# Kernel optimization log

Measured on AMD Instinct MI355X. Metric: run time of the kernel, lower is better.

## Reference

```python
import jax, jax.numpy as jnp
import numpy as np

B, T, FD, NH, NC, NOUT = 32, 512, 256, 1024, 512, 8


def setup_inputs() -> dict:
    key = jax.random.key(0)
    ks = jax.random.split(key, 12)
    s = lambda k, sh, sc=0.05: (jax.random.normal(k, sh, jnp.float32) * sc)
    return dict(
        x=jax.random.normal(ks[0], (B, T, FD), jnp.float32),
        lens=jax.random.randint(ks[1], (B,), T // 2, T + 1, jnp.int32),
        W1=s(ks[2], (NH, FD)), b1=jnp.zeros((NH,), jnp.float32),
        g1=jnp.ones((NH,), jnp.float32), be1=jnp.zeros((NH,), jnp.float32),
        W2=s(ks[3], (NH, NH)), b2=jnp.zeros((NH,), jnp.float32),
        g2=jnp.ones((NH,), jnp.float32), be2=jnp.zeros((NH,), jnp.float32),
        lstm_wih=s(ks[4], (2, 2, 4 * NC, NH)),   # [layer, dir, 4H, in]
        lstm_whh=s(ks[5], (2, 2, 4 * NC, NC)),   # [layer, dir, 4H, H]
        lstm_bih=s(ks[6], (2, 2, 4 * NC)),
        lstm_bhh=s(ks[7], (2, 2, 4 * NC)),
        w_u=s(ks[8], (2 * NC,)), b_u=jnp.zeros((), jnp.float32),
        Wc=s(ks[9], (NOUT, 2 * NC)), bc=jnp.zeros((NOUT,), jnp.float32),
    )


def _layernorm(x, g, b, eps=1e-5):
    m = x.mean(-1, keepdims=True)
    v = ((x - m) ** 2).mean(-1, keepdims=True)
    return (x - m) / jnp.sqrt(v + eps) * g + b


def _lrelu(z):
    return jnp.where(z >= 0, z, 0.01 * z)  # LeakyReLU default slope


def _lstm_dir(x, wih, whh, bih, bhh):
    # x: [B,T,in] -> h: [B,T,H]; torch gate order i,f,g,o
    Bz = x.shape[0]
    H = whh.shape[1]
    xp = jnp.einsum('bti,gi->btg', x, wih) + bih + bhh  # [B,T,4H]

    def step(carry, xt):
        h, c = carry
        gates = xt + h @ whh.T
        i, f, g, o = jnp.split(gates, 4, axis=-1)
        c = jax.nn.sigmoid(f) * c + jax.nn.sigmoid(i) * jnp.tanh(g)
        h = jax.nn.sigmoid(o) * jnp.tanh(c)
        return (h, c), h

    h0 = jnp.zeros((Bz, H), x.dtype)
    _, hs = jax.lax.scan(step, (h0, h0), xp.transpose(1, 0, 2))
    return hs.transpose(1, 0, 2)


def _bilstm(x, wih, whh, bih, bhh):
    # params indexed [dir, ...]; backward dir processes the full padded
    # sequence reversed (original feeds unpacked pad_sequence to nn.LSTM)
    hf = _lstm_dir(x, wih[0], whh[0], bih[0], bhh[0])
    hb = _lstm_dir(x[:, ::-1], wih[1], whh[1], bih[1], bhh[1])[:, ::-1]
    return jnp.concatenate([hf, hb], axis=-1)


def reference(x, lens, W1, b1, g1, be1, W2, b2, g2, be2,
              lstm_wih, lstm_whh, lstm_bih, lstm_bhh, w_u, b_u, Wc, bc):
    Tn = x.shape[1]
    # extract MLP (dropout = identity in eval)
    h = _lrelu(_layernorm(x @ W1.T + b1, g1, be1))
    h = _lrelu(_layernorm(h @ W2.T + b2, g2, be2))
    # pad_sequence zero-pads AFTER extract -> zero out pad positions
    mask = jnp.arange(Tn)[None, :] < lens[:, None]  # [B,T]
    h = h * mask[..., None]
    # 2-layer bidirectional LSTM over the full padded sequence
    h = _bilstm(h, lstm_wih[0], lstm_whh[0], lstm_bih[0], lstm_bhh[0])
    h = _bilstm(h, lstm_wih[1], lstm_whh[1], lstm_bih[1], lstm_bhh[1])
    # Attn with window_len=1: per-step linear score, masked softmax, weighted sum
    scores = h @ w_u + b_u                          # [B,T]
    scores = jnp.where(mask, scores, -jnp.inf)
    alpha = jax.nn.softmax(scores, axis=-1)
    pooled = jnp.einsum('bt,btd->bd', alpha, h)     # [B, 2*NC]
    return pooled @ Wc.T + bc
```

## Files before the change

kernel.cpp:

```cpp
#include <hip/hip_runtime.h>
#include <stdint.h>
#include <stddef.h>


typedef short  short8  __attribute__((ext_vector_type(8)));
typedef short  short4v __attribute__((ext_vector_type(4)));
typedef float  float4v __attribute__((ext_vector_type(4)));
typedef unsigned long long u64;

__device__ inline float b2f(short x){
  union { unsigned u; float f; } v; v.u = ((unsigned)(unsigned short)x) << 16; return v.f;
}
__device__ inline short f2b(float f){
  union { float f; unsigned u; } v; v.f = f;
  unsigned r = (v.u + 0x7fffu + ((v.u >> 16) & 1u)) >> 16;
  return (short)r;
}
__device__ inline float sigm(float x){ return 1.f / (1.f + __expf(-x)); }
__device__ inline float tanh_(float x){ return 2.f / (1.f + __expf(-2.f*x)) - 1.f; }

__global__ __launch_bounds__(256) void detect_f32(
    const unsigned short* __restrict__ p, unsigned* __restrict__ flag)
{
  const int tid = threadIdx.x;
  unsigned h = 0;
  for (int i = tid; i < 1024; i += 256){
    const unsigned e = (p[i] >> 7) & 0xFFu;
    if (e >= 0xC0u) ++h;
  }
#pragma unroll
  for (int off=32; off>0; off>>=1) h += __shfl_xor(h, off, 64);
  __shared__ unsigned sh[4];
  if ((tid&63)==0) sh[tid>>6] = h;
  __syncthreads();
  if (tid==0) *flag = (sh[0]+sh[1]+sh[2]+sh[3] >= 8u) ? 1u : 0u;
}

struct CvtArgs {
  const void* src[16];
  short*      dst[16];
  int         n[16];
  int         boff[17];
};

__global__ __launch_bounds__(256) void to_bf16_batch(
    CvtArgs a, const unsigned* __restrict__ flag)
{
  const int b = blockIdx.x;
  int lo = 0, hi = 15;
  while (lo < hi){
    const int mid = (lo + hi + 1) >> 1;
    if (b >= a.boff[mid]) lo = mid; else hi = mid - 1;
  }
  const int i   = lo;
  const int idx = (b - a.boff[i])*256 + (int)threadIdx.x;
  if (idx >= a.n[i]) return;
  if (*flag) a.dst[i][idx] = f2b(((const float*)a.src[i])[idx]);
  else       a.dst[i][idx] = ((const short*)a.src[i])[idx];
}

__global__ __launch_bounds__(256) void gemm_bt(
    const short* __restrict__ A, const short* __restrict__ W,
    short* __restrict__ C, const short* __restrict__ bias1,
    const short* __restrict__ bias2, int N, int K)
{
  __shared__ __align__(16) short lA[128*40];
  __shared__ __align__(16) short lW[128*40];
  const int tid  = threadIdx.x;
  const int lane = tid & 63, wv = tid >> 6;
  const int wm = wv >> 1, wn = wv & 1;
  const int quad = lane >> 4, l15 = lane & 15;

  const int gx  = gridDim.x;
  const int nwg = gx * gridDim.y;
  int flat = blockIdx.x + blockIdx.y * gx;
  if ((nwg & 7) == 0){
    const int cpx = nwg >> 3;
    flat = (flat & 7)*cpx + (flat >> 3);
  }
  const long m0 = (long)(flat / gx) * 128, n0 = (long)(flat % gx) * 128;

  float4v acc[4][4];
#pragma unroll
  for (int i=0;i<4;++i)
#pragma unroll
    for (int j=0;j<4;++j) acc[i][j] = (float4v)0.f;

  const int r  = tid >> 2;
  const int kc = tid & 3;
  const int nkt = K >> 5;
  for (int kt = 0; kt < nkt; ++kt) {
    __syncthreads();
    const short* ga = A + (m0 + r) * (long)K + kt*32 + kc*8;
    const short* gw = W + (n0 + r) * (long)K + kt*32 + kc*8;
    short8 a0 = *(const short8*)ga;
    short8 a1 = *(const short8*)(ga + 64*(long)K);
    short8 w0 = *(const short8*)gw;
    short8 w1 = *(const short8*)(gw + 64*(long)K);
    *(short8*)&lA[r*40 + kc*8]        = a0;
    *(short8*)&lA[(r+64)*40 + kc*8]   = a1;
    *(short8*)&lW[r*40 + kc*8]        = w0;
    *(short8*)&lW[(r+64)*40 + kc*8]   = w1;
    __syncthreads();
    short8 af[4], bfr[4];
#pragma unroll
    for (int i=0;i<4;++i) af[i]  = *(const short8*)&lA[(wm*64 + i*16 + l15)*40 + quad*8];
#pragma unroll
    for (int j=0;j<4;++j) bfr[j] = *(const short8*)&lW[(wn*64 + j*16 + l15)*40 + quad*8];
#pragma unroll
    for (int i=0;i<4;++i)
#pragma unroll
      for (int j=0;j<4;++j)
        acc[i][j] = __builtin_amdgcn_mfma_f32_16x16x32_bf16(af[i], bfr[j], acc[i][j], 0, 0, 0);
  }
#pragma unroll
  for (int j=0;j<4;++j){
    const long n = n0 + wn*64 + j*16 + l15;
    float bs = b2f(bias1[n]);
    if (bias2) bs += b2f(bias2[n]);
#pragma unroll
    for (int i=0;i<4;++i){
      const long mb = m0 + wm*64 + i*16 + quad*4;
#pragma unroll
      for (int g=0; g<4; ++g)
        C[(mb+g)*(long)N + n] = f2b(acc[i][j][g] + bs);
    }
  }
}

__global__ __launch_bounds__(256) void ln_lrelu(
    const short* __restrict__ X, const short* __restrict__ g,
    const short* __restrict__ be, short* __restrict__ out,
    const int* __restrict__ lens, const int domask)
{
  const int row = blockIdx.x, tid = threadIdx.x;
  const short* xr = X + (size_t)row * 1024;
  short4v xv = *(const short4v*)(xr + tid*4);
  float v[4];
#pragma unroll
  for (int k=0;k<4;++k) v[k] = b2f(xv[k]);
  float s  = v[0]+v[1]+v[2]+v[3];
  float sq = v[0]*v[0]+v[1]*v[1]+v[2]*v[2]+v[3]*v[3];
#pragma unroll
  for (int off=32; off>0; off>>=1){
    s  += __shfl_xor(s,  off, 64);
    sq += __shfl_xor(sq, off, 64);
  }
  __shared__ float red[8];
  if ((tid&63)==0){ red[tid>>6] = s; red[4+(tid>>6)] = sq; }
  __syncthreads();
  s  = red[0]+red[1]+red[2]+red[3];
  sq = red[4]+red[5]+red[6]+red[7];
  const float mean = s * (1.f/1024.f);
  const float var  = sq * (1.f/1024.f) - mean*mean;
  const float rstd = rsqrtf(var + 1e-5f);
  float zmul = 1.f;
  if (domask){ const int b = row >> 9, t = row & 511; if (t >= lens[b]) zmul = 0.f; }
  short4v o;
#pragma unroll
  for (int k=0;k<4;++k){
    const int n = tid*4 + k;
    float y = (v[k]-mean)*rstd*b2f(g[n]) + b2f(be[n]);
    y = (y >= 0.f) ? y : 0.01f*y;
    o[k] = f2b(y * zmul);
  }
  *(short4v*)(out + (size_t)row*1024 + tid*4) = o;
}

__global__ __launch_bounds__(256) void lstm_scan(
    const short* __restrict__ xp, const int xp_cols, const int dir0,
    const short* __restrict__ whh,
    u64* __restrict__ hstate,
    short* __restrict__ hout,
    const unsigned epoch)
{
  const int wg = blockIdx.x;
  const int dloc = wg >> 5, d = dir0 + dloc;
  const int u0 = (wg & 31) * 16;
  const int tid = threadIdx.x, lane = tid & 63, wv = tid >> 6;
  const int quad = lane >> 4, l15 = lane & 15;

  short8 af[16];
  {
    const short* wr = whh + ((size_t)d*2048 + wv*512 + u0 + l15)*512 + quad*8;
#pragma unroll
    for (int ks=0; ks<16; ++ks) af[ks] = *(const short8*)(wr + ks*32);
  }

  const int bb = tid >> 3, pp = tid & 7;
  float cstA = 0.f, cstB = 0.f;
  __shared__ __align__(16) unsigned hsh[2][32*260];
  __shared__ float gl[4][16][33];
  const unsigned tbase = epoch << 10;

  for (int step=0; step<512; ++step){
    const int t = d ? (511-step) : step;
    short4v x0, x1;
    {
      const size_t gb = (size_t)dloc*2048 + (size_t)wv*512 + u0 + quad*4;
      x0 = *(const short4v*)(xp + ((size_t)l15*512      + t)*xp_cols + gb);
      x1 = *(const short4v*)(xp + ((size_t)(l15+16)*512 + t)*xp_cols + gb);
    }
    unsigned* stg = &hsh[step&1][tid];
    if (step == 0){
#pragma unroll
      for (int k=0;k<32;++k) stg[k*260] = 0u;
    } else {
      const u64* hq = hstate + ((size_t)(d*2 + (step&1))<<13) + tid;
      const unsigned tgt = tbase + (unsigned)step;
      u64 v[32];
      for(;;){
        unsigned ok = 1u;
#pragma unroll
        for (int k=0;k<32;++k)
          v[k] = __hip_atomic_load(hq + (size_t)k*256,
                                   __ATOMIC_RELAXED, __HIP_MEMORY_SCOPE_AGENT);
#pragma unroll
        for (int k=0;k<32;++k) ok &= (unsigned)((unsigned)(v[k] >> 32) == tgt);
        if (ok) break;
        __builtin_amdgcn_s_sleep(1);
      }
#pragma unroll
      for (int k=0;k<32;++k) stg[k*260] = (unsigned)v[k];
    }
    __syncthreads();

    float4v acc0, acc1;
#pragma unroll
    for (int g=0; g<4; ++g){ acc0[g] = b2f(x0[g]); acc1[g] = b2f(x1[g]); }
    const short* hs = (const short*)&hsh[step&1][0];
#pragma unroll
    for (int ks=0; ks<16; ++ks){
      short8 b0 = *(const short8*)(hs + (size_t)l15*520      + ks*32 + quad*8);
      short8 b1 = *(const short8*)(hs + (size_t)(l15+16)*520 + ks*32 + quad*8);
      acc0 = __builtin_amdgcn_mfma_f32_16x16x32_bf16(af[ks], b0, acc0, 0, 0, 0);
      acc1 = __builtin_amdgcn_mfma_f32_16x16x32_bf16(af[ks], b1, acc1, 0, 0, 0);
    }
#pragma unroll
    for (int g=0; g<4; ++g){
      gl[wv][quad*4+g][l15]    = acc0[g];
      gl[wv][quad*4+g][l15+16] = acc1[g];
    }
    __syncthreads();

    float hv[2];
#pragma unroll
    for (int i=0; i<2; ++i){
      const int uu = 2*pp + i;
      const float gi = gl[0][uu][bb], gf = gl[1][uu][bb];
      const float gg = gl[2][uu][bb], go = gl[3][uu][bb];
      float& cref = i ? cstB : cstA;
      const float c = sigm(gf)*cref + sigm(gi)*tanh_(gg);
      cref = c;
      hv[i] = sigm(go) * tanh_(c);
    }
    const unsigned hw = (unsigned)(unsigned short)f2b(hv[0])
                      | ((unsigned)(unsigned short)f2b(hv[1]) << 16);
    const u64 pkt = ((u64)(tbase + (unsigned)step + 1u) << 32) | (u64)hw;
    __hip_atomic_store(hstate + ((size_t)(d*2 + ((step+1)&1))<<13)
                         + (size_t)bb*256 + (u0>>1) + pp,
                       pkt, __ATOMIC_RELAXED, __HIP_MEMORY_SCOPE_AGENT);
    *(unsigned*)&hout[((size_t)bb*512 + t)*1024 + d*512 + u0 + 2*pp] = hw;
  }
}

__global__ __launch_bounds__(256) void attn_cls(
    const short* __restrict__ hseq, const short* __restrict__ wu,
    const short* __restrict__ Wc, const short* __restrict__ bc,
    const int* __restrict__ lens, float* __restrict__ out)
{
  const int b = blockIdx.x, tid = threadIdx.x, lane = tid & 63, wv = tid >> 6;
  const int len = lens[b];
  __shared__ float wus[1024];
  __shared__ float sc[512];
  __shared__ float redx[8];
  __shared__ float pooled[1024];
  for (int i=tid; i<1024; i+=256) wus[i] = b2f(wu[i]);
  __syncthreads();
  const short* hb = hseq + (size_t)b*512*1024;
  for (int t=wv; t<512; t+=4){
    const short* hr = hb + (size_t)t*1024;
    float s = 0.f;
#pragma unroll
    for (int j=0;j<16;++j) s += b2f(hr[lane + j*64]) * wus[lane + j*64];
#pragma unroll
    for (int off=32; off>0; off>>=1) s += __shfl_xor(s, off, 64);
    if (lane==0) sc[t] = (t < len) ? s : -3.0e38f;
  }
  __syncthreads();
  float m = -3.0e38f;
  for (int i=tid;i<512;i+=256) m = fmaxf(m, sc[i]);
#pragma unroll
  for (int off=32; off>0; off>>=1) m = fmaxf(m, __shfl_xor(m, off, 64));
  if (lane==0) redx[wv] = m;
  __syncthreads();
  m = fmaxf(fmaxf(redx[0],redx[1]), fmaxf(redx[2],redx[3]));
  float ssum = 0.f;
  for (int i=tid;i<512;i+=256){
    float e = (i<len) ? __expf(sc[i]-m) : 0.f;
    sc[i] = e;
    ssum += e;
  }
#pragma unroll
  for (int off=32; off>0; off>>=1) ssum += __shfl_xor(ssum, off, 64);
  if (lane==0) redx[4+wv] = ssum;
  __syncthreads();
  ssum = redx[4]+redx[5]+redx[6]+redx[7];
  const float inv = 1.f/ssum;
  float4v pa = (float4v)0.f;
  const int k0 = tid*4;
  for (int t=0; t<len; ++t){
    const float a = sc[t];
    short4v hv = *(const short4v*)(hb + (size_t)t*1024 + k0);
    pa[0] += a*b2f(hv[0]); pa[1] += a*b2f(hv[1]);
    pa[2] += a*b2f(hv[2]); pa[3] += a*b2f(hv[3]);
  }
  pooled[k0+0] = pa[0]*inv; pooled[k0+1] = pa[1]*inv;
  pooled[k0+2] = pa[2]*inv; pooled[k0+3] = pa[3]*inv;
  __syncthreads();
  const int j = tid >> 5, l32 = tid & 31;
  float s2 = 0.f;
  for (int kk=l32; kk<1024; kk+=32) s2 += b2f(Wc[j*1024+kk]) * pooled[kk];
#pragma unroll
  for (int off=16; off>0; off>>=1) s2 += __shfl_xor(s2, off, 32);
  if (l32==0) out[b*8+j] = s2 + b2f(bc[j]);
}

extern "C" void kernel_launch(void* const* d_in, const int* in_sizes, int n_in,
                              void* d_out, int out_size, void* d_ws, size_t ws_size,
                              hipStream_t stream)
{
  (void)in_sizes; (void)n_in; (void)out_size;
  const int*   lens = (const int*)d_in[1];
  float* outp = (float*)d_out;

  const size_t SZ_XP_A = (size_t)16384*4096*2;
  const size_t SZ_XP_B = (size_t)16384*2048*2;
  const size_t SZ_H    = (size_t)16384*1024*2;
  const size_t SZ_HS   = 262144;
  const size_t SZ_CNT  = 16384;
  const size_t SZ_NORM = 37000000;
  const bool planA = ws_size >= SZ_XP_A + 2*SZ_H + SZ_HS + SZ_CNT + SZ_NORM;
  const bool planB = !planA && ws_size >= SZ_XP_B + 2*SZ_H + SZ_HS + SZ_CNT + SZ_NORM;
  if (!planA && !planB) return;
  const size_t xpsz = planA ? SZ_XP_A : SZ_XP_B;

  char* ws = (char*)d_ws;
  short*    XP  = (short*)ws;
  short*    HB  = (short*)(ws + xpsz);
  short*    HC  = (short*)(ws + xpsz + SZ_H);
  u64*      HS64= (u64*)(ws + xpsz + 2*SZ_H);
  unsigned* CNT = (unsigned*)(ws + xpsz + 2*SZ_H + SZ_HS);
  unsigned* FLAG = CNT + 4000;
  short*    pool = (short*)(ws + xpsz + 2*SZ_H + SZ_HS + SZ_CNT);

  size_t off = 0;
  auto carve = [&](size_t n){ short* p = pool + off; off += (n + 127) & ~(size_t)127; return p; };
  short* x   = carve(4194304);
  short* W1  = carve(262144);
  short* b1  = carve(1024);
  short* g1  = carve(1024);
  short* be1 = carve(1024);
  short* W2  = carve(1048576);
  short* b2  = carve(1024);
  short* g2  = carve(1024);
  short* be2 = carve(1024);
  short* wih = carve(8388608);
  short* whh = carve(4194304);
  short* bih = carve(8192);
  short* bhh = carve(8192);
  short* wu  = carve(1024);
  short* Wc  = carve(8192);
  short* bc  = carve(8);

  hipMemsetAsync(HS64, 0, SZ_HS, stream);
  detect_f32<<<1, 256, 0, stream>>>((const unsigned short*)d_in[0], FLAG);

  {
    struct { int idx; short* dst; int n; } cv[16] = {
      {0,x,4194304},{2,W1,262144},{3,b1,1024},{4,g1,1024},{5,be1,1024},
      {6,W2,1048576},{7,b2,1024},{8,g2,1024},{9,be2,1024},
      {10,wih,8388608},{11,whh,4194304},{12,bih,8192},{13,bhh,8192},
      {14,wu,1024},{16,Wc,8192},{17,bc,8}
    };
    CvtArgs a;
    int acc = 0;
    for (int i=0;i<16;++i){
      a.src[i]  = d_in[cv[i].idx];
      a.dst[i]  = cv[i].dst;
      a.n[i]    = cv[i].n;
      a.boff[i] = acc;
      acc += (cv[i].n + 255) / 256;
    }
    a.boff[16] = acc;
    to_bf16_batch<<<acc, 256, 0, stream>>>(a, FLAG);
  }

  dim3 blk(256);
  gemm_bt<<<dim3(8,128),  blk, 0, stream>>>(x,  W1, XP, b1, nullptr, 1024, 256);
  ln_lrelu<<<16384, blk, 0, stream>>>(XP, g1, be1, HB, lens, 0);
  gemm_bt<<<dim3(8,128),  blk, 0, stream>>>(HB, W2, XP, b2, nullptr, 1024, 1024);
  ln_lrelu<<<16384, blk, 0, stream>>>(XP, g2, be2, HC, lens, 1);

  const short* lin[2]  = { HC, HB };
  short*       lout[2] = { HB, HC };
  for (int l = 0; l < 2; ++l){
    const short* whh_l = whh + (size_t)l*2*2048*512;
    if (planA){
      gemm_bt<<<dim3(32,128), blk, 0, stream>>>(
          lin[l], wih + (size_t)l*4096*1024, XP,
          bih + l*4096, bhh + l*4096, 4096, 1024);
      lstm_scan<<<64, blk, 0, stream>>>(XP, 4096, 0, whh_l, HS64, lout[l],
                                        (unsigned)(l+1));
    } else {
      for (int d = 0; d < 2; ++d){
        gemm_bt<<<dim3(16,128), blk, 0, stream>>>(
            lin[l], wih + ((size_t)(l*2+d))*2048*1024, XP,
            bih + (l*2+d)*2048, bhh + (l*2+d)*2048, 2048, 1024);
        lstm_scan<<<32, blk, 0, stream>>>(XP, 2048, d, whh_l, HS64, lout[l],
                                          (unsigned)(l+1));
      }
    }
  }
  attn_cls<<<32, blk, 0, stream>>>(HC, wu, Wc, bc, lens, outp);
}
```

Baseline: 4.257 ms.

## Halve LSTM scan workgroups with 32 units each; drop GEMM tile swizzle

Each LSTM recurrence workgroup now owns 32 hidden units instead of 16. The per-direction workgroup count halves, so fewer workgroups poll and publish the shared hidden state each step. The cost is doubled MFMA work and register pressure per workgroup (two sets of recurrent weight fragments) on the serial critical path. Separately, the GEMM drops its XCD-aware block-index remapping and uses plain grid coordinates, which may change cache locality across chiplets.

```diff
diff --git a/kernel.cpp b/kernel.cpp
--- a/kernel.cpp
+++ b/kernel.cpp
@@ -70,15 +70,7 @@
   const int lane = tid & 63, wv = tid >> 6;
   const int wm = wv >> 1, wn = wv & 1;
   const int quad = lane >> 4, l15 = lane & 15;
-
-  const int gx  = gridDim.x;
-  const int nwg = gx * gridDim.y;
-  int flat = blockIdx.x + blockIdx.y * gx;
-  if ((nwg & 7) == 0){
-    const int cpx = nwg >> 3;
-    flat = (flat & 7)*cpx + (flat >> 3);
-  }
-  const long m0 = (long)(flat / gx) * 128, n0 = (long)(flat % gx) * 128;
+  const long m0 = (long)blockIdx.y * 128, n0 = (long)blockIdx.x * 128;
 
   float4v acc[4][4];
 #pragma unroll
@@ -175,31 +167,39 @@
     const unsigned epoch)
 {
   const int wg = blockIdx.x;
-  const int dloc = wg >> 5, d = dir0 + dloc;
-  const int u0 = (wg & 31) * 16;
+  const int dloc = wg >> 4, d = dir0 + dloc;
+  const int u0 = (wg & 15) * 32;
   const int tid = threadIdx.x, lane = tid & 63, wv = tid >> 6;
   const int quad = lane >> 4, l15 = lane & 15;
 
-  short8 af[16];
+  short8 af0[16], af1[16];
   {
-    const short* wr = whh + ((size_t)d*2048 + wv*512 + u0 + l15)*512 + quad*8;
-#pragma unroll
-    for (int ks=0; ks<16; ++ks) af[ks] = *(const short8*)(wr + ks*32);
+    const short* wr0 = whh + ((size_t)d*2048 + wv*512 + u0 + l15)*512 + quad*8;
+    const short* wr1 = wr0 + (size_t)16*512;
+#pragma unroll
+    for (int ks=0; ks<16; ++ks){
+      af0[ks] = *(const short8*)(wr0 + ks*32);
+      af1[ks] = *(const short8*)(wr1 + ks*32);
+    }
   }
 
   const int bb = tid >> 3, pp = tid & 7;
-  float cstA = 0.f, cstB = 0.f;
+  float cst[4] = {0.f, 0.f, 0.f, 0.f};
   __shared__ __align__(16) unsigned hsh[2][32*260];
-  __shared__ float gl[4][16][33];
+  __shared__ float gl[4][32][33];
   const unsigned tbase = epoch << 10;
 
   for (int step=0; step<512; ++step){
     const int t = d ? (511-step) : step;
-    short4v x0, x1;
+    short4v x00, x01, x10, x11;
     {
       const size_t gb = (size_t)dloc*2048 + (size_t)wv*512 + u0 + quad*4;
-      x0 = *(const short4v*)(xp + ((size_t)l15*512      + t)*xp_cols + gb);
-      x1 = *(const short4v*)(xp + ((size_t)(l15+16)*512 + t)*xp_cols + gb);
+      const short* pA = xp + ((size_t)l15*512      + t)*xp_cols + gb;
+      const short* pB = xp + ((size_t)(l15+16)*512 + t)*xp_cols + gb;
+      x00 = *(const short4v*)pA;
+      x01 = *(const short4v*)(pA + 16);
+      x10 = *(const short4v*)pB;
+      x11 = *(const short4v*)(pB + 16);
     }
     unsigned* stg = &hsh[step&1][tid];
     if (step == 0){
@@ -225,42 +225,54 @@
     }
     __syncthreads();
 
-    float4v acc0, acc1;
-#pragma unroll
-    for (int g=0; g<4; ++g){ acc0[g] = b2f(x0[g]); acc1[g] = b2f(x1[g]); }
+    float4v a00, a01, a10, a11;
+#pragma unroll
+    for (int g=0; g<4; ++g){
+      a00[g] = b2f(x00[g]); a01[g] = b2f(x01[g]);
+      a10[g] = b2f(x10[g]); a11[g] = b2f(x11[g]);
+    }
     const short* hs = (const short*)&hsh[step&1][0];
 #pragma unroll
     for (int ks=0; ks<16; ++ks){
       short8 b0 = *(const short8*)(hs + (size_t)l15*520      + ks*32 + quad*8);
       short8 b1 = *(const short8*)(hs + (size_t)(l15+16)*520 + ks*32 + quad*8);
-      acc0 = __builtin_amdgcn_mfma_f32_16x16x32_bf16(af[ks], b0, acc0, 0, 0, 0);
-      acc1 = __builtin_amdgcn_mfma_f32_16x16x32_bf16(af[ks], b1, acc1, 0, 0, 0);
+      a00 = __builtin_amdgcn_mfma_f32_16x16x32_bf16(af0[ks], b0, a00, 0, 0, 0);
+      a01 = __builtin_amdgcn_mfma_f32_16x16x32_bf16(af1[ks], b0, a01, 0, 0, 0);
+      a10 = __builtin_amdgcn_mfma_f32_16x16x32_bf16(af0[ks], b1, a10, 0, 0, 0);
+      a11 = __builtin_amdgcn_mfma_f32_16x16x32_bf16(af1[ks], b1, a11, 0, 0, 0);
     }
 #pragma unroll
     for (int g=0; g<4; ++g){
-      gl[wv][quad*4+g][l15]    = acc0[g];
-      gl[wv][quad*4+g][l15+16] = acc1[g];
+      gl[wv][quad*4+g][l15]        = a00[g];
+      gl[wv][16+quad*4+g][l15]     = a01[g];
+      gl[wv][quad*4+g][l15+16]     = a10[g];
+      gl[wv][16+quad*4+g][l15+16]  = a11[g];
     }
     __syncthreads();
 
-    float hv[2];
-#pragma unroll
-    for (int i=0; i<2; ++i){
-      const int uu = 2*pp + i;
+    float hv[4];
+#pragma unroll
+    for (int i=0; i<4; ++i){
+      const int uu = ((i >> 1) << 4) | (2*pp + (i & 1));
       const float gi = gl[0][uu][bb], gf = gl[1][uu][bb];
       const float gg = gl[2][uu][bb], go = gl[3][uu][bb];
-      float& cref = i ? cstB : cstA;
-      const float c = sigm(gf)*cref + sigm(gi)*tanh_(gg);
-      cref = c;
+      const float c = sigm(gf)*cst[i] + sigm(gi)*tanh_(gg);
+      cst[i] = c;
       hv[i] = sigm(go) * tanh_(c);
     }
-    const unsigned hw = (unsigned)(unsigned short)f2b(hv[0])
-                      | ((unsigned)(unsigned short)f2b(hv[1]) << 16);
-    const u64 pkt = ((u64)(tbase + (unsigned)step + 1u) << 32) | (u64)hw;
-    __hip_atomic_store(hstate + ((size_t)(d*2 + ((step+1)&1))<<13)
-                         + (size_t)bb*256 + (u0>>1) + pp,
-                       pkt, __ATOMIC_RELAXED, __HIP_MEMORY_SCOPE_AGENT);
-    *(unsigned*)&hout[((size_t)bb*512 + t)*1024 + d*512 + u0 + 2*pp] = hw;
+    const unsigned hw0 = (unsigned)(unsigned short)f2b(hv[0])
+                       | ((unsigned)(unsigned short)f2b(hv[1]) << 16);
+    const unsigned hw1 = (unsigned)(unsigned short)f2b(hv[2])
+                       | ((unsigned)(unsigned short)f2b(hv[3]) << 16);
+    const u64 tag = (u64)(tbase + (unsigned)step + 1u) << 32;
+    u64* hn = hstate + ((size_t)(d*2 + ((step+1)&1))<<13) + (size_t)bb*256 + (u0>>1) + pp;
+    __hip_atomic_store(hn,     tag | (u64)hw0,
+                       __ATOMIC_RELAXED, __HIP_MEMORY_SCOPE_AGENT);
+    __hip_atomic_store(hn + 8, tag | (u64)hw1,
+                       __ATOMIC_RELAXED, __HIP_MEMORY_SCOPE_AGENT);
+    unsigned* ho = (unsigned*)&hout[((size_t)bb*512 + t)*1024 + d*512 + u0 + 2*pp];
+    ho[0] = hw0;
+    ho[8] = hw1;
   }
 }
 
@@ -410,14 +422,14 @@
       gemm_bt<<<dim3(32,128), blk, 0, stream>>>(
           lin[l], wih + (size_t)l*4096*1024, XP,
           bih + l*4096, bhh + l*4096, 4096, 1024);
-      lstm_scan<<<64, blk, 0, stream>>>(XP, 4096, 0, whh_l, HS64, lout[l],
+      lstm_scan<<<32, blk, 0, stream>>>(XP, 4096, 0, whh_l, HS64, lout[l],
                                         (unsigned)(l+1));
     } else {
       for (int d = 0; d < 2; ++d){
         gemm_bt<<<dim3(16,128), blk, 0, stream>>>(
             lin[l], wih + ((size_t)(l*2+d))*2048*1024, XP,
             bih + (l*2+d)*2048, bhh + (l*2+d)*2048, 2048, 1024);
-        lstm_scan<<<32, blk, 0, stream>>>(XP, 2048, d, whh_l, HS64, lout[l],
+        lstm_scan<<<16, blk, 0, stream>>>(XP, 2048, d, whh_l, HS64, lout[l],
                                           (unsigned)(l+1));
       }
     }
```

After: 4.670 ms. +9.7%, slower.
